# Optimization experiments

Hardware: AMD Instinct MI355X
Metric: run time of the kernel (lower is better)

The kernel has to match this reference:

```python
import jax, jax.numpy as jnp
import numpy as np

DIM = 1024
N_HEADS = 16
HEAD_DIM = DIM // N_HEADS


def setup_inputs() -> dict:
    key = jax.random.key(0)
    ks = jax.random.split(key, 6)
    s = DIM ** -0.5
    return {
        "x": jax.random.normal(ks[0], (2, 2048, DIM), dtype=jnp.float32),
        "Wq": jax.random.normal(ks[1], (DIM, DIM), dtype=jnp.float32) * s,
        "Wk": jax.random.normal(ks[2], (DIM, DIM), dtype=jnp.float32) * s,
        "Wv": jax.random.normal(ks[3], (DIM, DIM), dtype=jnp.float32) * s,
        "Wo": jax.random.normal(ks[4], (DIM, DIM), dtype=jnp.float32) * s,
        "bo": jax.random.normal(ks[5], (DIM,), dtype=jnp.float32) * 0.01,
    }


def reference(x, Wq, Wk, Wv, Wo, bo):
    B, T, C = x.shape
    H, D = N_HEADS, HEAD_DIM
    # Linear(dim, dim, bias=False): y = x @ W^T
    q = (x @ Wq.T).reshape(B, T, H, D).transpose(0, 2, 1, 3)  # B H T D
    k = (x @ Wk.T).reshape(B, T, H, D).transpose(0, 2, 1, 3)
    v = (x @ Wv.T).reshape(B, T, H, D).transpose(0, 2, 1, 3)
    q = q * (D ** -0.5)
    attn = jnp.einsum('bhqd,bhkd->bhqk', q, k)  # B H T T
    causal_mask = jnp.triu(jnp.ones((T, T), dtype=bool), k=1)
    attn = jnp.where(causal_mask, -jnp.inf, attn)
    attn = jax.nn.softmax(attn, axis=-1)
    out = jnp.einsum('bhqk,bhkd->bhqd', attn, v)  # B H T D
    out = out.transpose(0, 2, 1, 3).reshape(B, T, C)
    return out @ Wo.T + bo
```

## Files before the change

### kernel.cpp

```cpp
#include <hip/hip_runtime.h>
#include <math.h>

typedef __attribute__((ext_vector_type(8))) short bf16x8;
typedef __attribute__((ext_vector_type(4))) float f32x4;
typedef __attribute__((ext_vector_type(16))) float f32x16;

__device__ __forceinline__ ushort f2bf(float f) {
  union { float f; unsigned u; } v; v.f = f;
  return (ushort)((v.u + 0x8000u) >> 16);
}

__device__ __forceinline__ void g2l16(const void* g, void* l) {
  __builtin_amdgcn_global_load_lds((const __attribute__((address_space(1))) unsigned*)g,
                                   (__attribute__((address_space(3))) unsigned*)l, 16, 0, 0);
}

__global__ __launch_bounds__(256) void cast_all(const float* __restrict__ x,
                                                const float* __restrict__ Wq,
                                                const float* __restrict__ Wk,
                                                const float* __restrict__ Wv,
                                                const float* __restrict__ Wo,
                                                ushort* __restrict__ xbf,
                                                ushort* __restrict__ wcat,
                                                float4* __restrict__ O32) {
  int i = blockIdx.x * 256 + threadIdx.x;
  if (i < 1048576) {
    float4 v = ((const float4*)x)[i];
    ushort4 u; u.x = f2bf(v.x); u.y = f2bf(v.y); u.z = f2bf(v.z); u.w = f2bf(v.w);
    ((ushort4*)xbf)[i] = u;
  } else if (i < 2097152) {
    int j = i - 1048576;
    int sel = j >> 18;
    const float* src = (sel == 0) ? Wq : (sel == 1) ? Wk : (sel == 2) ? Wv : Wo;
    float scale = (sel == 0) ? 0.125f * 1.44269504088896f : 1.0f;
    float4 v = ((const float4*)src)[j & 0x3FFFF];
    ushort4 u;
    u.x = f2bf(v.x * scale); u.y = f2bf(v.y * scale);
    u.z = f2bf(v.z * scale); u.w = f2bf(v.w * scale);
    ((ushort4*)wcat)[j] = u;
  } else {
    O32[i - 2097152] = float4{0.f, 0.f, 0.f, 0.f};
  }
}

__global__ __launch_bounds__(256) void gemm_qkv(const ushort* __restrict__ A,
                                                const ushort* __restrict__ B,
                                                ushort* __restrict__ C3,
                                                ushort* __restrict__ Vt) {
  const int K = 1024;
  __shared__ __align__(16) ushort smem[17408];
  ushort* As = smem;
  ushort* Bs = smem + 8192;
  const int m0 = blockIdx.y * 128, n0 = blockIdx.x * 128;
  const int tid = threadIdx.x, lane = tid & 63, wid = tid >> 6;
  const int quad = lane >> 4, lc = lane & 15;
  const int lrow = lane >> 2, lcol = (lane & 3) * 8;
  const int wm = (wid >> 1) * 64, wn = (wid & 1) * 64;

  f32x4 acc[4][4] = {};

  auto stage = [&](int k0, int nb) {
    const ushort* Ag = A + (size_t)(m0 + wid * 32 + lrow) * K + k0 + lcol;
    g2l16(Ag, &As[nb * 4096 + wid * 1024]);
    g2l16(Ag + (size_t)16 * K, &As[nb * 4096 + wid * 1024 + 512]);
    const ushort* Bg = B + (size_t)(n0 + wid * 32 + lrow) * K + k0 + lcol;
    g2l16(Bg, &Bs[nb * 4096 + wid * 1024]);
    g2l16(Bg + (size_t)16 * K, &Bs[nb * 4096 + wid * 1024 + 512]);
  };

  stage(0, 0);
  for (int k0 = 0; k0 < K; k0 += 32) {
    const int nb = (k0 >> 5) & 1;
    __syncthreads();
    if (k0 + 32 < K) stage(k0 + 32, nb ^ 1);

    bf16x8 af[4], bfr[4];
#pragma unroll
    for (int t = 0; t < 4; t++)
      af[t] = *(const bf16x8*)&As[nb * 4096 + (wm + t * 16 + lc) * 32 + quad * 8];
#pragma unroll
    for (int t = 0; t < 4; t++)
      bfr[t] = *(const bf16x8*)&Bs[nb * 4096 + (wn + t * 16 + lc) * 32 + quad * 8];
#pragma unroll
    for (int mt = 0; mt < 4; mt++)
#pragma unroll
      for (int nt = 0; nt < 4; nt++)
        acc[mt][nt] = __builtin_amdgcn_mfma_f32_16x16x32_bf16(af[mt], bfr[nt], acc[mt][nt], 0, 0, 0);
  }

  const int sel = n0 >> 10;
  if (sel < 2) {
#pragma unroll
    for (int mt = 0; mt < 4; mt++) {
#pragma unroll
      for (int r = 0; r < 4; r++) {
        int row = m0 + wm + mt * 16 + quad * 4 + r;
#pragma unroll
        for (int nt = 0; nt < 4; nt++) {
          int col = n0 + wn + nt * 16 + lc;
          size_t dst = ((size_t)sel << 22) + (size_t)row * 1024 + (col & 1023);
          C3[dst] = f2bf(acc[mt][nt][r]);
        }
      }
    }
  } else {
    __syncthreads();
#pragma unroll
    for (int mt = 0; mt < 4; mt++)
#pragma unroll
      for (int r = 0; r < 4; r++) {
        int tl = wm + mt * 16 + quad * 4 + r;
#pragma unroll
        for (int nt = 0; nt < 4; nt++)
          smem[(wn + nt * 16 + lc) * 136 + tl] = f2bf(acc[mt][nt][r]);
      }
    __syncthreads();
    const int hd0 = n0 - 2048, b = m0 >> 11, t_base = m0 & 2047;
#pragma unroll
    for (int i = 0; i < 8; i++) {
      int idx = i * 256 + tid;
      int dl = idx >> 4, tc = (idx & 15) * 8;
      uint4 v = *(const uint4*)&smem[dl * 136 + tc];
      int hd = hd0 + dl;
      *(uint4*)(Vt + (size_t)(b * 16 + (hd >> 6)) * 131072 +
                (size_t)(hd & 63) * 2048 + t_base + tc) = v;
    }
  }
}

__global__ __launch_bounds__(256) void gemm_proj(const ushort* __restrict__ A,
                                                 const ushort* __restrict__ B,
                                                 float* __restrict__ C,
                                                 const float* __restrict__ bias) {
  const int K = 1024;
  __shared__ __align__(16) ushort As[2][2][128 * 32];
  __shared__ __align__(16) ushort Bs[2][2][64 * 32];
  const int m0 = blockIdx.y * 128, n0 = blockIdx.x * 64;
  const int tid = threadIdx.x, lane = tid & 63, wid = tid >> 6;
  const int quad = lane >> 4, lc = lane & 15;
  const int lrow = lane >> 2, lcol = (lane & 3) * 8;
  const int wm = (wid >> 1) * 64, wn = (wid & 1) * 32;

  f32x4 acc[4][2] = {};

  auto stage = [&](int k0, int nb) {
    const ushort* Ag = A + (size_t)(m0 + wid * 32 + lrow) * K + k0 + lcol;
    g2l16(Ag,                       &As[nb][0][wid * 1024]);
    g2l16(Ag + (size_t)16 * K,      &As[nb][0][wid * 1024 + 512]);
    g2l16(Ag + 32,                  &As[nb][1][wid * 1024]);
    g2l16(Ag + (size_t)16 * K + 32, &As[nb][1][wid * 1024 + 512]);
    const ushort* Bg = B + (size_t)(n0 + wid * 16 + lrow) * K + k0 + lcol;
    g2l16(Bg,      &Bs[nb][0][wid * 512]);
    g2l16(Bg + 32, &Bs[nb][1][wid * 512]);
  };

  stage(0, 0);
  for (int k0 = 0; k0 < K; k0 += 64) {
    const int nb = (k0 >> 6) & 1;
    __syncthreads();
    if (k0 + 64 < K) stage(k0 + 64, nb ^ 1);

#pragma unroll
    for (int ks = 0; ks < 2; ks++) {
      bf16x8 af[4], bfr[2];
#pragma unroll
      for (int t = 0; t < 4; t++)
        af[t] = *(const bf16x8*)&As[nb][ks][(wm + t * 16 + lc) * 32 + quad * 8];
#pragma unroll
      for (int t = 0; t < 2; t++)
        bfr[t] = *(const bf16x8*)&Bs[nb][ks][(wn + t * 16 + lc) * 32 + quad * 8];
#pragma unroll
      for (int mt = 0; mt < 4; mt++)
#pragma unroll
        for (int nt = 0; nt < 2; nt++)
          acc[mt][nt] = __builtin_amdgcn_mfma_f32_16x16x32_bf16(af[mt], bfr[nt], acc[mt][nt], 0, 0, 0);
    }
  }

#pragma unroll
  for (int mt = 0; mt < 4; mt++) {
#pragma unroll
    for (int r = 0; r < 4; r++) {
      int row = m0 + wm + mt * 16 + quad * 4 + r;
#pragma unroll
      for (int nt = 0; nt < 2; nt++) {
        int col = n0 + wn + nt * 16 + lc;
        C[(size_t)row * 1024 + col] = acc[mt][nt][r] + bias[col];
      }
    }
  }
}

__global__ __launch_bounds__(256, 4) void attn_kernel(const ushort* __restrict__ Qb,
                                                      const ushort* __restrict__ Kb,
                                                      const ushort* __restrict__ Vt,
                                                      float* __restrict__ O32,
                                                      float* __restrict__ L32) {
  __shared__ __align__(16) ushort Ks[4096];
  __shared__ __align__(16) ushort Vs[4096];

  const int bh = blockIdx.x, b = bh >> 4, h = bh & 15;
  const int f = (int)blockIdx.y;
  int qi, ci;
  if (f < 16)      { qi = 12 + (f >> 2); ci = f & 3; }
  else if (f < 28) { int g = f - 16; int q3 = g / 3; qi = 8 + q3; ci = g - 3 * q3; }
  else if (f < 36) { int g = f - 28; qi = 4 + (g >> 1); ci = g & 1; }
  else             { qi = f - 36; ci = 0; }
  const int t0 = ci * 8;
  const int t1 = min(t0 + 8, 2 * qi + 2);

  const int tid = threadIdx.x, lane = tid & 63, wid = tid >> 6;
  const int hi = lane >> 5, ln = lane & 31;
  const int qbw = qi * 128 + wid * 32;
  const int qg = qbw + ln;

  const size_t kbase = (size_t)(b * 2048) * 1024 + h * 64;
  const size_t vbase = (size_t)bh * 131072;

  bf16x8 qf[4];
  {
    const ushort* Qp = Qb + kbase + (size_t)qg * 1024 + hi * 8;
#pragma unroll
    for (int dc = 0; dc < 4; dc++)
      qf[dc] = *(const bf16x8*)(Qp + dc * 16);
  }

  f32x16 o_acc[2] = {};
  float l_own = 0.f;

  const int krow = lane >> 3, kcol = lane & 7;
  const int dsw = (kcol ^ krow) << 3;
  const int shalf = wid & 1;

  auto stage = [&](int kb) {
    if (wid < 2) {
      const ushort* gK = Kb + kbase + (size_t)(kb + shalf * 32 + krow) * 1024 + dsw;
#pragma unroll
      for (int i = 0; i < 4; i++)
        g2l16(gK + (size_t)(i * 8) * 1024, &Ks[(shalf * 4 + i) * 512]);
    } else {
      const ushort* gV = Vt + vbase + (size_t)(shalf * 32 + krow) * 2048 + kb + dsw;
#pragma unroll
      for (int i = 0; i < 4; i++)
        g2l16(gV + (size_t)(i * 8) * 2048, &Vs[(shalf * 4 + i) * 512]);
    }
  };

  const int sx = ln & 7;

  for (int kt = t0; kt < t1; kt++) {
    const int kb = kt * 64;
    __builtin_amdgcn_s_barrier();
    stage(kb);
    asm volatile("s_waitcnt vmcnt(0)" ::: "memory");
    __builtin_amdgcn_s_barrier();

#pragma unroll
    for (int g64 = 0; g64 < 2; g64++) {
      if (kb + g64 * 32 > qbw + 31) continue;
      f32x16 s;
#pragma unroll
      for (int z = 0; z < 16; z++) s[z] = 0.f;
      __builtin_amdgcn_s_setprio(1);
#pragma unroll
      for (int dc = 0; dc < 4; dc++) {
        bf16x8 kf = *(const bf16x8*)&Ks[(g64 * 32 + ln) * 64 + (((dc * 2 + hi) ^ sx) << 3)];
        s = __builtin_amdgcn_mfma_f32_32x32x16_bf16(kf, qf[dc], s, 0, 0, 0);
      }
      __builtin_amdgcn_s_setprio(0);

      unsigned U[8];
      const bool dmask = (kb + g64 * 32 + 31 > qbw);
      if (dmask) {
        const int c = qg - kb - g64 * 32 - hi * 4;
#pragma unroll
        for (int g = 0; g < 4; g++) {
          float e[4];
#pragma unroll
          for (int j = 0; j < 4; j++) {
            float sv = s[g * 4 + j];
            if (g * 8 + j > c) sv = -1e30f;
            e[j] = __builtin_amdgcn_exp2f(sv);
          }
          l_own += (e[0] + e[1]) + (e[2] + e[3]);
          union { float f; unsigned u; } f0{e[0]}, f1{e[1]}, f2{e[2]}, f3{e[3]};
          U[g * 2]     = __builtin_amdgcn_perm(f1.u + 0x8000u, f0.u + 0x8000u, 0x07060302u);
          U[g * 2 + 1] = __builtin_amdgcn_perm(f3.u + 0x8000u, f2.u + 0x8000u, 0x07060302u);
        }
      } else {
#pragma unroll
        for (int g = 0; g < 4; g++) {
          float e[4];
#pragma unroll
          for (int j = 0; j < 4; j++)
            e[j] = __builtin_amdgcn_exp2f(s[g * 4 + j]);
          l_own += (e[0] + e[1]) + (e[2] + e[3]);
          union { float f; unsigned u; } f0{e[0]}, f1{e[1]}, f2{e[2]}, f3{e[3]};
          U[g * 2]     = __builtin_amdgcn_perm(f1.u + 0x8000u, f0.u + 0x8000u, 0x07060302u);
          U[g * 2 + 1] = __builtin_amdgcn_perm(f3.u + 0x8000u, f2.u + 0x8000u, 0x07060302u);
        }
      }

      __builtin_amdgcn_s_setprio(1);
#pragma unroll
      for (int half = 0; half < 2; half++) {
        const int m = g64 * 2 + half;
        bf16x8 pfrag;
#pragma unroll
        for (int w = 0; w < 4; w++) ((unsigned*)&pfrag)[w] = U[half * 4 + w];
#pragma unroll
        for (int dg = 0; dg < 2; dg++) {
          const ushort* vrow = &Vs[(dg * 32 + ln) * 64];
          bf16x8 vbf;
          *(unsigned long long*)&vbf =
              *(const unsigned long long*)&vrow[(((2 * m) ^ sx) << 3) + 4 * hi];
          *((unsigned long long*)&vbf + 1) =
              *(const unsigned long long*)&vrow[(((2 * m + 1) ^ sx) << 3) + 4 * hi];
          o_acc[dg] = __builtin_amdgcn_mfma_f32_32x32x16_bf16(pfrag, vbf, o_acc[dg], 0, 0, 0);
        }
      }
      __builtin_amdgcn_s_setprio(0);
    }
  }

  {
    float lt = l_own + __shfl_xor(l_own, 32);
    if (hi == 0) atomicAdd(&L32[(size_t)bh * 2048 + qg], lt);
  }
#pragma unroll
  for (int r = 0; r < 16; r++) {
    int q = qbw + (r & 3) + ((r >> 2) << 3) + hi * 4;
    size_t orow = ((size_t)(b * 2048) + q) * 1024 + h * 64 + ln;
    atomicAdd(&O32[orow], o_acc[0][r]);
    atomicAdd(&O32[orow + 32], o_acc[1][r]);
  }
}

__global__ __launch_bounds__(256) void normalize_kernel(const float* __restrict__ O32,
                                                        const float* __restrict__ L32,
                                                        ushort* __restrict__ Out) {
  const int row = blockIdx.x;
  const int tid = threadIdx.x;
  const int col = tid * 4;
  const int b = row >> 11, t = row & 2047, h = col >> 6;
  const float inv = 1.0f / L32[(size_t)(b * 16 + h) * 2048 + t];
  float4 o = ((const float4*)(O32 + (size_t)row * 1024))[tid];
  ushort4 u;
  u.x = f2bf(o.x * inv); u.y = f2bf(o.y * inv);
  u.z = f2bf(o.z * inv); u.w = f2bf(o.w * inv);
  ((ushort4*)(Out + (size_t)row * 1024))[tid] = u;
}

extern "C" void kernel_launch(void* const* d_in, const int* in_sizes, int n_in,
                              void* d_out, int out_size, void* d_ws, size_t ws_size,
                              hipStream_t stream) {
  const float* x  = (const float*)d_in[0];
  const float* Wq = (const float*)d_in[1];
  const float* Wk = (const float*)d_in[2];
  const float* Wv = (const float*)d_in[3];
  const float* Wo = (const float*)d_in[4];
  const float* bo = (const float*)d_in[5];
  float* out = (float*)d_out;

  char* ws = (char*)d_ws;
  ushort* xbf  = (ushort*)(ws);
  ushort* wcat = (ushort*)(ws + (8ull  << 20));
  ushort* qkv  = (ushort*)(ws + (16ull << 20));
  ushort* Qp   = qkv;
  ushort* Kp   = qkv + (1ull << 22);
  ushort* Vt   = qkv + (2ull << 22);
  float*  L32  = (float*)ws;
  float*  O32  = out;
  ushort* attn_out = Qp;

  cast_all<<<12288, 256, 0, stream>>>(x, Wq, Wk, Wv, Wo, xbf, wcat, (float4*)O32);

  gemm_qkv<<<dim3(24, 32), 256, 0, stream>>>(xbf, wcat, qkv, Vt);

  hipMemsetAsync(L32, 0, (size_t)32 * 2048 * 4, stream);

  attn_kernel<<<dim3(32, 40), 256, 0, stream>>>(Qp, Kp, Vt, O32, L32);

  normalize_kernel<<<4096, 256, 0, stream>>>(O32, L32, attn_out);

  gemm_proj<<<dim3(16, 32), 256, 0, stream>>>(
      attn_out, wcat + (size_t)3072 * 1024, out, bo);
}
```

Measured before the change: 196.9 us.

## Replace attention split-K atomics with per-chunk partial buffers reduced in normalize

Attention blocks no longer atomically add their unnormalized outputs into a zeroed fp32 buffer. Chunk 0 writes fp32 partials directly, and chunks 1-3 write bf16 partials into separate compact workspace buffers. The normalize kernel then sums whichever chunks exist for each row. This removes the zero-fill pass in the cast kernel and the contention and read-modify-write traffic of global float atomics. In exchange the bf16 partials lose some precision and the normalize kernel reads more data.

Measured after the change: 187.5 us. -4.8%, faster.

```diff
diff --git a/kernel.cpp b/kernel.cpp
--- a/kernel.cpp
+++ b/kernel.cpp
@@ -8,6 +8,10 @@
 __device__ __forceinline__ ushort f2bf(float f) {
   union { float f; unsigned u; } v; v.f = f;
   return (ushort)((v.u + 0x8000u) >> 16);
+}
+__device__ __forceinline__ float bf2f(ushort u) {
+  union { unsigned u; float f; } v; v.u = (unsigned)u << 16;
+  return v.f;
 }
 
 __device__ __forceinline__ void g2l16(const void* g, void* l) {
@@ -21,14 +25,13 @@
                                                 const float* __restrict__ Wv,
                                                 const float* __restrict__ Wo,
                                                 ushort* __restrict__ xbf,
-                                                ushort* __restrict__ wcat,
-                                                float4* __restrict__ O32) {
+                                                ushort* __restrict__ wcat) {
   int i = blockIdx.x * 256 + threadIdx.x;
   if (i < 1048576) {
     float4 v = ((const float4*)x)[i];
     ushort4 u; u.x = f2bf(v.x); u.y = f2bf(v.y); u.z = f2bf(v.z); u.w = f2bf(v.w);
     ((ushort4*)xbf)[i] = u;
-  } else if (i < 2097152) {
+  } else {
     int j = i - 1048576;
     int sel = j >> 18;
     const float* src = (sel == 0) ? Wq : (sel == 1) ? Wk : (sel == 2) ? Wv : Wo;
@@ -38,8 +41,6 @@
     u.x = f2bf(v.x * scale); u.y = f2bf(v.y * scale);
     u.z = f2bf(v.z * scale); u.w = f2bf(v.w * scale);
     ((ushort4*)wcat)[j] = u;
-  } else {
-    O32[i - 2097152] = float4{0.f, 0.f, 0.f, 0.f};
   }
 }
 
@@ -194,7 +195,10 @@
 __global__ __launch_bounds__(256, 4) void attn_kernel(const ushort* __restrict__ Qb,
                                                       const ushort* __restrict__ Kb,
                                                       const ushort* __restrict__ Vt,
-                                                      float* __restrict__ O32,
+                                                      float* __restrict__ S0,
+                                                      ushort* __restrict__ S1,
+                                                      ushort* __restrict__ S2,
+                                                      ushort* __restrict__ S3,
                                                       float* __restrict__ L32) {
   __shared__ __align__(16) ushort Ks[4096];
   __shared__ __align__(16) ushort Vs[4096];
@@ -327,24 +331,54 @@
     float lt = l_own + __shfl_xor(l_own, 32);
     if (hi == 0) atomicAdd(&L32[(size_t)bh * 2048 + qg], lt);
   }
-#pragma unroll
-  for (int r = 0; r < 16; r++) {
-    int q = qbw + (r & 3) + ((r >> 2) << 3) + hi * 4;
-    size_t orow = ((size_t)(b * 2048) + q) * 1024 + h * 64 + ln;
-    atomicAdd(&O32[orow], o_acc[0][r]);
-    atomicAdd(&O32[orow + 32], o_acc[1][r]);
-  }
-}
-
-__global__ __launch_bounds__(256) void normalize_kernel(const float* __restrict__ O32,
+  if (ci == 0) {
+#pragma unroll
+    for (int r = 0; r < 16; r++) {
+      int q = qbw + (r & 3) + ((r >> 2) << 3) + hi * 4;
+      size_t orow = ((size_t)(b * 2048) + q) * 1024 + h * 64 + ln;
+      S0[orow] = o_acc[0][r];
+      S0[orow + 32] = o_acc[1][r];
+    }
+  } else {
+    ushort* Sp = (ci == 1) ? S1 : (ci == 2) ? S2 : S3;
+    const int roff = (ci == 1) ? 512 : (ci == 2) ? 1024 : 1536;
+    const int rcnt = 2048 - roff;
+#pragma unroll
+    for (int r = 0; r < 16; r++) {
+      int q = qbw + (r & 3) + ((r >> 2) << 3) + hi * 4;
+      size_t srow = ((size_t)(b * rcnt) + (q - roff)) * 1024 + h * 64 + ln;
+      Sp[srow] = f2bf(o_acc[0][r]);
+      Sp[srow + 32] = f2bf(o_acc[1][r]);
+    }
+  }
+}
+
+__global__ __launch_bounds__(256) void normalize_kernel(const float* __restrict__ S0,
+                                                        const ushort* __restrict__ S1,
+                                                        const ushort* __restrict__ S2,
+                                                        const ushort* __restrict__ S3,
                                                         const float* __restrict__ L32,
                                                         ushort* __restrict__ Out) {
   const int row = blockIdx.x;
   const int tid = threadIdx.x;
   const int col = tid * 4;
   const int b = row >> 11, t = row & 2047, h = col >> 6;
+  const int qi = t >> 7;
+  const int nch = (2 * qi + 9) >> 3;
+  float4 o = ((const float4*)(S0 + (size_t)row * 1024))[tid];
+  if (nch > 1) {
+    ushort4 p = ((const ushort4*)(S1 + ((size_t)(b * 1536) + t - 512) * 1024))[tid];
+    o.x += bf2f(p.x); o.y += bf2f(p.y); o.z += bf2f(p.z); o.w += bf2f(p.w);
+  }
+  if (nch > 2) {
+    ushort4 p = ((const ushort4*)(S2 + ((size_t)(b * 1024) + t - 1024) * 1024))[tid];
+    o.x += bf2f(p.x); o.y += bf2f(p.y); o.z += bf2f(p.z); o.w += bf2f(p.w);
+  }
+  if (nch > 3) {
+    ushort4 p = ((const ushort4*)(S3 + ((size_t)(b * 512) + t - 1536) * 1024))[tid];
+    o.x += bf2f(p.x); o.y += bf2f(p.y); o.z += bf2f(p.z); o.w += bf2f(p.w);
+  }
   const float inv = 1.0f / L32[(size_t)(b * 16 + h) * 2048 + t];
-  float4 o = ((const float4*)(O32 + (size_t)row * 1024))[tid];
   ushort4 u;
   u.x = f2bf(o.x * inv); u.y = f2bf(o.y * inv);
   u.z = f2bf(o.z * inv); u.w = f2bf(o.w * inv);
@@ -369,19 +403,22 @@
   ushort* Qp   = qkv;
   ushort* Kp   = qkv + (1ull << 22);
   ushort* Vt   = qkv + (2ull << 22);
-  float*  L32  = (float*)ws;
-  float*  O32  = out;
+  ushort* S1   = (ushort*)(ws);
+  ushort* S2   = (ushort*)(ws + (6ull  << 20));
+  ushort* S3   = (ushort*)(ws + (10ull << 20));
+  float*  L32  = (float*)(ws + (12ull << 20));
+  float*  S0   = out;
   ushort* attn_out = Qp;
 
-  cast_all<<<12288, 256, 0, stream>>>(x, Wq, Wk, Wv, Wo, xbf, wcat, (float4*)O32);
+  cast_all<<<8192, 256, 0, stream>>>(x, Wq, Wk, Wv, Wo, xbf, wcat);
 
   gemm_qkv<<<dim3(24, 32), 256, 0, stream>>>(xbf, wcat, qkv, Vt);
 
   hipMemsetAsync(L32, 0, (size_t)32 * 2048 * 4, stream);
 
-  attn_kernel<<<dim3(32, 40), 256, 0, stream>>>(Qp, Kp, Vt, O32, L32);
-
-  normalize_kernel<<<4096, 256, 0, stream>>>(O32, L32, attn_out);
+  attn_kernel<<<dim3(32, 40), 256, 0, stream>>>(Qp, Kp, Vt, S0, S1, S2, S3, L32);
+
+  normalize_kernel<<<4096, 256, 0, stream>>>(S0, S1, S2, S3, L32, attn_out);
 
   gemm_proj<<<dim3(16, 32), 256, 0, stream>>>(
       attn_out, wcat + (size_t)3072 * 1024, out, bo);
```
